# Kernel optimization log

Hardware: AMD Instinct MI355X
Metric: run time of the kernel (lower is better)

Reference implementation:

```python
import jax, jax.numpy as jnp
import numpy as np
import math

B, H, W = 32, 512, 512
BS = 8
QUALITY = 50.0  # __scale_quality(75) = 200 - 2*75


def _make_dctmtx(bs=BS):
    m = np.empty((bs, bs), dtype=np.float32)
    for j in range(bs):
        for i in range(bs):
            if i == 0:
                m[i, j] = 1.0 / math.sqrt(bs)
            else:
                m[i, j] = math.sqrt(2.0 / bs) * math.cos(math.pi * (2 * j + 1) * i / (2 * bs))
    return jnp.asarray(m)


def _make_quantize():
    qY = np.array([[16,11,10,16,24,40,51,61],[12,12,14,19,26,58,60,55],
                   [14,13,16,24,40,57,69,56],[14,17,22,29,51,87,80,62],
                   [18,22,37,56,68,109,103,77],[24,35,55,64,81,104,113,92],
                   [49,64,78,87,103,121,120,101],[72,92,95,98,112,100,103,99]], dtype=np.float32) / 255.0
    qC = np.array([[17,18,24,47,99,99,99,99],[18,21,26,66,99,99,99,99],
                   [24,26,56,99,99,99,99,99],[47,66,99,99,99,99,99,99],
                   [99,99,99,99,99,99,99,99],[99,99,99,99,99,99,99,99],
                   [99,99,99,99,99,99,99,99],[99,99,99,99,99,99,99,99]], dtype=np.float32) / 255.0
    return jnp.asarray(np.stack([qY, qC, qC], axis=0))


def setup_inputs() -> dict:
    key = jax.random.key(0)
    x = jax.random.uniform(key, (B, 3, H, W), dtype=jnp.float32)
    return {"input": x, "quantize": _make_quantize(), "dctmtx": _make_dctmtx()}


def reference(input, quantize, dctmtx):
    bs = BS
    b, c, h, w = input.shape
    dt = input.dtype
    rgb = 255.0 * input
    # rgb -> ycbcr (3x3 color transform, offset cb/cr by 128, clamp)
    xf = jnp.array([[0.299, 0.587, 0.114],
                    [-0.168735892, -0.331264108, 0.5],
                    [0.5, -0.418687589, -0.081312411]], dtype=dt)
    off = jnp.array([0.0, 128.0, 128.0], dtype=dt)[None, :, None, None]
    ycbcr = jnp.clip(jnp.einsum('bchw,kc->bkhw', rgb, xf) + off, 0.0, 255.0)
    # 2x2 chroma subsample: replace Cb/Cr by 2x2 block means (Y untouched)
    yc = ycbcr[:, :1]
    cc = ycbcr[:, 1:].reshape(b, 2, h // 2, 2, w // 2, 2)
    cm = jnp.mean(cc, axis=(3, 5), keepdims=True)
    cc = jnp.broadcast_to(cm, cc.shape).reshape(b, 2, h, w)
    sample = jnp.concatenate([yc, cc], axis=1) - 128.0
    # extract 8x8 blocks -> [b, h/bs, w/bs, 3, bs, bs]
    blocks = sample.reshape(b, 3, h // bs, bs, w // bs, bs).transpose(0, 2, 4, 1, 3, 5)
    # 2D DCT: D @ X @ D^T
    dcts = jnp.einsum('ij,bhwcjk,lk->bhwcil', dctmtx, blocks, dctmtx)
    # quality-scaled quant table (broadcasts [3,8,8] over blocks)
    q = jnp.round(jnp.clip(jnp.round((jnp.round(quantize * 255.0) * QUALITY + 50.0) / 100.0), 1.0, 255.0))
    comp = jnp.round(dcts / q)
    decomp = jnp.round(comp * jax.lax.stop_gradient(q))
    # IDCT: D^T @ X @ D
    idcts = jnp.einsum('ji,bhwcjk,kl->bhwcil', dctmtx, decomp, dctmtx)
    # merge blocks back -> [b,3,h,w]
    ycbcr2 = idcts.transpose(0, 3, 1, 4, 2, 5).reshape(b, 3, h, w) + 128.0
    # ycbcr -> rgb
    xf2 = jnp.array([[1.0, 0.0, 1.402],
                     [1.0, -0.344136286, -0.714136286],
                     [1.0, 1.772, 0.0]], dtype=dt)
    im = ycbcr2 - off
    rgb2 = jnp.clip(jnp.einsum('bchw,kc->bkhw', im, xf2), 0.0, 255.0)
    return jnp.round(rgb2) / 255.0
```

## Files before the change

kernel.cpp:

```cpp
#include <hip/hip_runtime.h>

#define IN_H 512
#define IN_W 512


__global__ __launch_bounds__(256, 2) void jpeg_kernel(
    const float* __restrict__ in, const float* __restrict__ qz,
    const float* __restrict__ dmtx, float* __restrict__ out)
{
    __shared__ __align__(16) unsigned char smem[62592];
    double* Ys   = (double*)(smem);
    double* CbS  = (double*)(smem + 16512);
    double* CrS  = (double*)(smem + 24832);
    double* T    = (double*)(smem + 33152);
    float*  U    = (float*) (smem + 33152);
    float*  Z    = (float*) (smem + 50560);
    double* qtab = (double*)(smem + 59264);
    float*  Df   = (float*) (smem + 62336);
    float* V[3]  = { (float*)(smem), (float*)(smem + 16512), (float*)(smem + 24832) };

    const int t   = threadIdx.x;
    const int blk = blockIdx.x;
    const int b   = blk >> 7;
    const int rr  = blk & 127;
    const int row0 = (rr >> 1) << 3;
    const int col0 = (rr & 1) << 8;
    const int chs = IN_H * IN_W;

    if (t < 192) {
        double v  = (double)qz[t];
        double t0 = rint(v * 255.0);
        double t1 = rint((t0 * 50.0 + 50.0) / 100.0);
        double q  = fmin(fmax(t1, 1.0), 255.0);
        qtab[2*t]   = 1.0 / q;
        qtab[2*t+1] = q;
    }
    if (t < 64) Df[t] = dmtx[t];

    const int s  = t >> 6;
    const int c4 = t & 63;
    {
        const int base = ((b*3) * IN_H + row0 + 2*s) * IN_W + col0 + 4*c4;
        float4 ra = *(const float4*)(in + base);
        float4 rb = *(const float4*)(in + base + IN_W);
        float4 ga = *(const float4*)(in + base + chs);
        float4 gb = *(const float4*)(in + base + chs + IN_W);
        float4 ba = *(const float4*)(in + base + 2*chs);
        float4 bb = *(const float4*)(in + base + 2*chs + IN_W);

        float rA[2][4] = {{ra.x,ra.y,ra.z,ra.w},{rb.x,rb.y,rb.z,rb.w}};
        float gA[2][4] = {{ga.x,ga.y,ga.z,ga.w},{gb.x,gb.y,gb.z,gb.w}};
        float bA[2][4] = {{ba.x,ba.y,ba.z,ba.w},{bb.x,bb.y,bb.z,bb.w}};

        double yv[2][4], cbv[2][4], crv[2][4];
        #pragma unroll
        for (int p = 0; p < 2; ++p) {
            #pragma unroll
            for (int k = 0; k < 4; ++k) {
                double R = 255.0 * (double)rA[p][k];
                double G = 255.0 * (double)gA[p][k];
                double B = 255.0 * (double)bA[p][k];
                double y  =  0.299*R + 0.587*G + 0.114*B;
                double cb = -0.168735892*R - 0.331264108*G + 0.5*B + 128.0;
                double cr =  0.5*R - 0.418687589*G - 0.081312411*B + 128.0;
                yv[p][k]  = fmin(fmax(y , 0.0), 255.0) - 128.0;
                cbv[p][k] = fmin(fmax(cb, 0.0), 255.0);
                crv[p][k] = fmin(fmax(cr, 0.0), 255.0);
            }
        }
        #pragma unroll
        for (int p = 0; p < 2; ++p) {
            double* yp = &Ys[(2*s+p)*258 + 4*c4];
            *(double2*)(yp)     = make_double2(yv[p][0], yv[p][1]);
            *(double2*)(yp + 2) = make_double2(yv[p][2], yv[p][3]);
        }
        double m0 = (cbv[0][0]+cbv[0][1]+cbv[1][0]+cbv[1][1])*0.25 - 128.0;
        double m1 = (cbv[0][2]+cbv[0][3]+cbv[1][2]+cbv[1][3])*0.25 - 128.0;
        *(double2*)&CbS[s*130 + 2*c4] = make_double2(m0, m1);
        double n0 = (crv[0][0]+crv[0][1]+crv[1][0]+crv[1][1])*0.25 - 128.0;
        double n1 = (crv[0][2]+crv[0][3]+crv[1][2]+crv[1][3])*0.25 - 128.0;
        *(double2*)&CrS[s*130 + 2*c4] = make_double2(n0, n1);
    }
    __syncthreads();

    float  dh[8][4];
    double dh64[8][4];
    #pragma unroll
    for (int l = 0; l < 8; ++l) {
        float4 d4 = *(const float4*)&Df[l*8];
        dh[l][0]=d4.x; dh[l][1]=d4.y; dh[l][2]=d4.z; dh[l][3]=d4.w;
        #pragma unroll
        for (int k = 0; k < 4; ++k) dh64[l][k] = (double)dh[l][k];
    }
    const int q8 = t >> 3;
    const int jl = t & 7;

    #pragma unroll
    for (int c = 0; c < 3; ++c) {
        {
            double x[8];
            if (c == 0) {
                const double* p = &Ys[jl*258 + q8*8];
                double2 a0 = *(const double2*)(p);
                double2 a1 = *(const double2*)(p+2);
                double2 a2 = *(const double2*)(p+4);
                double2 a3 = *(const double2*)(p+6);
                x[0]=a0.x; x[1]=a0.y; x[2]=a1.x; x[3]=a1.y;
                x[4]=a2.x; x[5]=a2.y; x[6]=a3.x; x[7]=a3.y;
            } else {
                const double* p = (c==1 ? CbS : CrS) + (jl>>1)*130 + q8*4;
                double2 a0 = *(const double2*)(p);
                double2 a1 = *(const double2*)(p+2);
                x[0]=a0.x; x[1]=a0.x; x[2]=a0.y; x[3]=a0.y;
                x[4]=a1.x; x[5]=a1.x; x[6]=a1.y; x[7]=a1.y;
            }
            double e[4], o[4];
            #pragma unroll
            for (int k = 0; k < 4; ++k) { e[k]=x[k]+x[7-k]; o[k]=x[k]-x[7-k]; }
            double* Tp = &T[q8*68 + jl*8];
            #pragma unroll
            for (int l = 0; l < 8; l += 2) {
                double te = dh64[l  ][0]*e[0] + dh64[l  ][1]*e[1] + dh64[l  ][2]*e[2] + dh64[l  ][3]*e[3];
                double to = dh64[l+1][0]*o[0] + dh64[l+1][1]*o[1] + dh64[l+1][2]*o[2] + dh64[l+1][3]*o[3];
                *(double2*)(Tp + l) = make_double2(te, to);
            }
        }
        __syncthreads();

        {
            const double* Tc = &T[q8*68 + jl];
            double tc[8];
            #pragma unroll
            for (int j2 = 0; j2 < 8; ++j2) tc[j2] = Tc[j2*8];
            double e2[4], o2[4];
            #pragma unroll
            for (int m = 0; m < 4; ++m) { e2[m]=tc[m]+tc[7-m]; o2[m]=tc[m]-tc[7-m]; }
            float* Zc = &Z[q8*68 + jl];
            #pragma unroll
            for (int i = 0; i < 8; ++i) {
                double acc;
                if ((i & 1) == 0)
                    acc = dh64[i][0]*e2[0]+dh64[i][1]*e2[1]+dh64[i][2]*e2[2]+dh64[i][3]*e2[3];
                else
                    acc = dh64[i][0]*o2[0]+dh64[i][1]*o2[1]+dh64[i][2]*o2[2]+dh64[i][3]*o2[3];
                double2 qe = *(const double2*)&qtab[2*(c*64 + i*8 + jl)];
                double comp = rint(acc * qe.x);
                Zc[i*8] = (float)(comp * qe.y);
            }
        }
        __syncthreads();

        {
            const float* Zp = &Z[q8*68 + jl*8];
            float4 z0 = *(const float4*)(Zp);
            float4 z1 = *(const float4*)(Zp+4);
            float zz[8] = {z0.x,z0.y,z0.z,z0.w,z1.x,z1.y,z1.z,z1.w};
            float se[4], so[4], uu[8];
            #pragma unroll
            for (int l2 = 0; l2 < 4; ++l2) {
                se[l2] = zz[0]*dh[0][l2] + zz[2]*dh[2][l2] + zz[4]*dh[4][l2] + zz[6]*dh[6][l2];
                so[l2] = zz[1]*dh[1][l2] + zz[3]*dh[3][l2] + zz[5]*dh[5][l2] + zz[7]*dh[7][l2];
            }
            #pragma unroll
            for (int l2 = 0; l2 < 4; ++l2) { uu[l2]=se[l2]+so[l2]; uu[7-l2]=se[l2]-so[l2]; }
            float* Upp = &U[q8*68 + jl*8];
            *(float4*)(Upp)   = make_float4(uu[0],uu[1],uu[2],uu[3]);
            *(float4*)(Upp+4) = make_float4(uu[4],uu[5],uu[6],uu[7]);
        }
        __syncthreads();

        {
            const float* Up2 = &U[q8*68 + jl];
            float uu[8];
            #pragma unroll
            for (int j2 = 0; j2 < 8; ++j2) uu[j2] = Up2[j2*8];
            float se[4], so[4];
            #pragma unroll
            for (int i2 = 0; i2 < 4; ++i2) {
                se[i2] = uu[0]*dh[0][i2] + uu[2]*dh[2][i2] + uu[4]*dh[4][i2] + uu[6]*dh[6][i2];
                so[i2] = uu[1]*dh[1][i2] + uu[3]*dh[3][i2] + uu[5]*dh[5][i2] + uu[7]*dh[7][i2];
            }
            float* Vc = V[c];
            #pragma unroll
            for (int i2 = 0; i2 < 4; ++i2) {
                Vc[i2*260     + q8*8 + jl] = se[i2] + so[i2];
                Vc[(7-i2)*260 + q8*8 + jl] = se[i2] - so[i2];
            }
        }
        __syncthreads();
    }

    {
        const int obase = ((b*3) * IN_H + row0 + 2*s) * IN_W + col0 + 4*c4;
        #pragma unroll
        for (int p = 0; p < 2; ++p) {
            const int roff = (2*s+p)*260 + 4*c4;
            float4 vy = *(const float4*)&V[0][roff];
            float4 vb = *(const float4*)&V[1][roff];
            float4 vr = *(const float4*)&V[2][roff];
            float yv2[4]={vy.x,vy.y,vy.z,vy.w};
            float cb2[4]={vb.x,vb.y,vb.z,vb.w};
            float cr2[4]={vr.x,vr.y,vr.z,vr.w};
            float R4[4],G4[4],B4[4];
            #pragma unroll
            for (int k = 0; k < 4; ++k) {
                float im0 = yv2[k] + 128.0f;
                float im1 = cb2[k];
                float im2 = cr2[k];
                float R = fminf(fmaxf(im0 + 1.402f*im2, 0.0f), 255.0f);
                float G = fminf(fmaxf(im0 - 0.344136286f*im1 - 0.714136286f*im2, 0.0f), 255.0f);
                float B = fminf(fmaxf(im0 + 1.772f*im1, 0.0f), 255.0f);
                R4[k] = rintf(R) * (1.0f/255.0f);
                G4[k] = rintf(G) * (1.0f/255.0f);
                B4[k] = rintf(B) * (1.0f/255.0f);
            }
            float* op = out + obase + p*IN_W;
            *(float4*)(op)         = make_float4(R4[0],R4[1],R4[2],R4[3]);
            *(float4*)(op + chs)   = make_float4(G4[0],G4[1],G4[2],G4[3]);
            *(float4*)(op + 2*chs) = make_float4(B4[0],B4[1],B4[2],B4[3]);
        }
    }
}

extern "C" void kernel_launch(void* const* d_in, const int* in_sizes, int n_in,
                              void* d_out, int out_size, void* d_ws, size_t ws_size,
                              hipStream_t stream) {
    (void)in_sizes; (void)n_in; (void)out_size; (void)d_ws; (void)ws_size;
    const float* in  = (const float*)d_in[0];
    const float* qz  = (const float*)d_in[1];
    const float* dm  = (const float*)d_in[2];
    float* out = (float*)d_out;
    dim3 grid(4096), blk(256);
    hipLaunchKernelGGL(jpeg_kernel, grid, blk, 0, stream, in, qz, dm, out);
}
```

Before: 195.3 us.

## Restructure JPEG DCT pipeline to cut shared memory and barriers, raise occupancy

```diff
diff --git a/kernel.cpp b/kernel.cpp
--- a/kernel.cpp
+++ b/kernel.cpp
@@ -4,20 +4,18 @@
 #define IN_W 512
 
 
-__global__ __launch_bounds__(256, 2) void jpeg_kernel(
+__global__ __launch_bounds__(256, 4) void jpeg_kernel(
     const float* __restrict__ in, const float* __restrict__ qz,
     const float* __restrict__ dmtx, float* __restrict__ out)
 {
-    __shared__ __align__(16) unsigned char smem[62592];
-    double* Ys   = (double*)(smem);
-    double* CbS  = (double*)(smem + 16512);
-    double* CrS  = (double*)(smem + 24832);
-    double* T    = (double*)(smem + 33152);
-    float*  U    = (float*) (smem + 33152);
-    float*  Z    = (float*) (smem + 50560);
-    double* qtab = (double*)(smem + 59264);
-    float*  Df   = (float*) (smem + 62336);
-    float* V[3]  = { (float*)(smem), (float*)(smem + 16512), (float*)(smem + 24832) };
+    __shared__ __align__(16) unsigned char smem[39168];
+    double*  Ys  = (double*) (smem);
+    double*  CbS = (double*) (smem + 17408);
+    double*  CrS = (double*) (smem + 22016);
+    float*   Zt  = (float*)  (smem + 26624);
+    double2* qt  = (double2*)(smem + 35328);
+    double*  Dd  = (double*) (smem + 38784);
+    float*   Dh  = (float*)  (smem + 39040);
 
     const int t   = threadIdx.x;
     const int blk = blockIdx.x;
@@ -28,25 +26,28 @@
     const int chs = IN_H * IN_W;
 
     if (t < 192) {
+        const int c = t >> 6, i = (t >> 3) & 7, l = t & 7;
         double v  = (double)qz[t];
-        double t0 = rint(v * 255.0);
-        double t1 = rint((t0 * 50.0 + 50.0) / 100.0);
+        double t1 = rint((rint(v * 255.0) * 50.0 + 50.0) / 100.0);
         double q  = fmin(fmax(t1, 1.0), 255.0);
-        qtab[2*t]   = 1.0 / q;
-        qtab[2*t+1] = q;
-    }
-    if (t < 64) Df[t] = dmtx[t];
+        qt[(c * 8 + l) * 9 + i] = make_double2(1.0 / q, q);
+    }
+    if (t < 32) {
+        float dv = dmtx[(t >> 2) * 8 + (t & 3)];
+        Dd[t] = (double)dv;
+        Dh[t] = dv;
+    }
 
     const int s  = t >> 6;
     const int c4 = t & 63;
     {
-        const int base = ((b*3) * IN_H + row0 + 2*s) * IN_W + col0 + 4*c4;
+        const int base = ((b * 3) * IN_H + row0 + 2 * s) * IN_W + col0 + 4 * c4;
         float4 ra = *(const float4*)(in + base);
         float4 rb = *(const float4*)(in + base + IN_W);
         float4 ga = *(const float4*)(in + base + chs);
         float4 gb = *(const float4*)(in + base + chs + IN_W);
-        float4 ba = *(const float4*)(in + base + 2*chs);
-        float4 bb = *(const float4*)(in + base + 2*chs + IN_W);
+        float4 ba = *(const float4*)(in + base + 2 * chs);
+        float4 bb = *(const float4*)(in + base + 2 * chs + IN_W);
 
         float rA[2][4] = {{ra.x,ra.y,ra.z,ra.w},{rb.x,rb.y,rb.z,rb.w}};
         float gA[2][4] = {{ga.x,ga.y,ga.z,ga.w},{gb.x,gb.y,gb.z,gb.w}};
@@ -68,157 +69,131 @@
                 crv[p][k] = fmin(fmax(cr, 0.0), 255.0);
             }
         }
+        const int tile = c4 >> 1, half = c4 & 1;
         #pragma unroll
         for (int p = 0; p < 2; ++p) {
-            double* yp = &Ys[(2*s+p)*258 + 4*c4];
+            double* yp = &Ys[tile * 68 + (2*s + p) * 8 + 4 * half];
             *(double2*)(yp)     = make_double2(yv[p][0], yv[p][1]);
             *(double2*)(yp + 2) = make_double2(yv[p][2], yv[p][3]);
         }
         double m0 = (cbv[0][0]+cbv[0][1]+cbv[1][0]+cbv[1][1])*0.25 - 128.0;
         double m1 = (cbv[0][2]+cbv[0][3]+cbv[1][2]+cbv[1][3])*0.25 - 128.0;
-        *(double2*)&CbS[s*130 + 2*c4] = make_double2(m0, m1);
+        *(double2*)&CbS[tile * 18 + s * 4 + 2 * half] = make_double2(m0, m1);
         double n0 = (crv[0][0]+crv[0][1]+crv[1][0]+crv[1][1])*0.25 - 128.0;
         double n1 = (crv[0][2]+crv[0][3]+crv[1][2]+crv[1][3])*0.25 - 128.0;
-        *(double2*)&CrS[s*130 + 2*c4] = make_double2(n0, n1);
+        *(double2*)&CrS[tile * 18 + s * 4 + 2 * half] = make_double2(n0, n1);
     }
     __syncthreads();
 
-    float  dh[8][4];
-    double dh64[8][4];
-    #pragma unroll
-    for (int l = 0; l < 8; ++l) {
-        float4 d4 = *(const float4*)&Df[l*8];
-        dh[l][0]=d4.x; dh[l][1]=d4.y; dh[l][2]=d4.z; dh[l][3]=d4.w;
-        #pragma unroll
-        for (int k = 0; k < 4; ++k) dh64[l][k] = (double)dh[l][k];
-    }
     const int q8 = t >> 3;
-    const int jl = t & 7;
+    const int l  = t & 7;
+    double dl0, dl1, dl2, dl3;
+    {
+        double2 dA = *(const double2*)&Dd[l * 4];
+        double2 dB = *(const double2*)&Dd[l * 4 + 2];
+        dl0 = dA.x; dl1 = dA.y; dl2 = dB.x; dl3 = dB.y;
+    }
+    const double sgn  = (l & 1) ? -1.0 : 1.0;
+    const double dl01 = dl0 + dl1, dl23 = dl2 + dl3;
+    float dcol[8];
+    {
+        const int   lc = (l < 4) ? l : 7 - l;
+        #pragma unroll
+        for (int k = 0; k < 8; ++k) {
+            float dv = Dh[k * 4 + lc];
+            dcol[k] = ((k & 1) && (l >= 4)) ? -dv : dv;
+        }
+    }
+
+    float acc[3][8];
 
     #pragma unroll
     for (int c = 0; c < 3; ++c) {
-        {
-            double x[8];
-            if (c == 0) {
-                const double* p = &Ys[jl*258 + q8*8];
+        double tj[8];
+        if (c == 0) {
+            const double* base = &Ys[q8 * 68];
+            #pragma unroll
+            for (int j = 0; j < 8; ++j) {
+                const double* p = base + j * 8;
                 double2 a0 = *(const double2*)(p);
-                double2 a1 = *(const double2*)(p+2);
-                double2 a2 = *(const double2*)(p+4);
-                double2 a3 = *(const double2*)(p+6);
-                x[0]=a0.x; x[1]=a0.y; x[2]=a1.x; x[3]=a1.y;
-                x[4]=a2.x; x[5]=a2.y; x[6]=a3.x; x[7]=a3.y;
-            } else {
-                const double* p = (c==1 ? CbS : CrS) + (jl>>1)*130 + q8*4;
-                double2 a0 = *(const double2*)(p);
-                double2 a1 = *(const double2*)(p+2);
-                x[0]=a0.x; x[1]=a0.x; x[2]=a0.y; x[3]=a0.y;
-                x[4]=a1.x; x[5]=a1.x; x[6]=a1.y; x[7]=a1.y;
+                double2 a1 = *(const double2*)(p + 2);
+                double2 a2 = *(const double2*)(p + 4);
+                double2 a3 = *(const double2*)(p + 6);
+                double v0 = fma(sgn, a3.y, a0.x);
+                double v1 = fma(sgn, a3.x, a0.y);
+                double v2 = fma(sgn, a2.y, a1.x);
+                double v3 = fma(sgn, a2.x, a1.y);
+                tj[j] = dl0*v0 + dl1*v1 + dl2*v2 + dl3*v3;
             }
-            double e[4], o[4];
+        } else {
+            const double* base = ((c == 1) ? CbS : CrS) + q8 * 18;
             #pragma unroll
-            for (int k = 0; k < 4; ++k) { e[k]=x[k]+x[7-k]; o[k]=x[k]-x[7-k]; }
-            double* Tp = &T[q8*68 + jl*8];
-            #pragma unroll
-            for (int l = 0; l < 8; l += 2) {
-                double te = dh64[l  ][0]*e[0] + dh64[l  ][1]*e[1] + dh64[l  ][2]*e[2] + dh64[l  ][3]*e[3];
-                double to = dh64[l+1][0]*o[0] + dh64[l+1][1]*o[1] + dh64[l+1][2]*o[2] + dh64[l+1][3]*o[3];
-                *(double2*)(Tp + l) = make_double2(te, to);
+            for (int j2 = 0; j2 < 4; ++j2) {
+                double2 a0 = *(const double2*)(base + j2 * 4);
+                double2 a1 = *(const double2*)(base + j2 * 4 + 2);
+                double u = dl01 * fma(sgn, a1.y, a0.x) + dl23 * fma(sgn, a1.x, a0.y);
+                tj[2*j2] = u; tj[2*j2 + 1] = u;
             }
         }
+        double e2[4], o2[4];
+        #pragma unroll
+        for (int m = 0; m < 4; ++m) { e2[m] = tj[m] + tj[7-m]; o2[m] = tj[m] - tj[7-m]; }
+
+        float zo[8];
+        const double2* dd2  = (const double2*)Dd;
+        const double2* qrow = &qt[(c * 8 + l) * 9];
+        #pragma unroll
+        for (int i = 0; i < 8; ++i) {
+            double2 dA = dd2[i * 2], dB = dd2[i * 2 + 1];
+            double a64 = (i & 1)
+                ? dA.x*o2[0] + dA.y*o2[1] + dB.x*o2[2] + dB.y*o2[3]
+                : dA.x*e2[0] + dA.y*e2[1] + dB.x*e2[2] + dB.y*e2[3];
+            double2 qe = qrow[i];
+            zo[i] = (float)(rint(a64 * qe.x) * qe.y);
+        }
+        float* zp = &Zt[q8 * 68 + l * 8];
+        *(float4*)(zp)     = make_float4(zo[0], zo[1], zo[2], zo[3]);
+        *(float4*)(zp + 4) = make_float4(zo[4], zo[5], zo[6], zo[7]);
         __syncthreads();
 
-        {
-            const double* Tc = &T[q8*68 + jl];
-            double tc[8];
-            #pragma unroll
-            for (int j2 = 0; j2 < 8; ++j2) tc[j2] = Tc[j2*8];
-            double e2[4], o2[4];
-            #pragma unroll
-            for (int m = 0; m < 4; ++m) { e2[m]=tc[m]+tc[7-m]; o2[m]=tc[m]-tc[7-m]; }
-            float* Zc = &Z[q8*68 + jl];
-            #pragma unroll
-            for (int i = 0; i < 8; ++i) {
-                double acc;
-                if ((i & 1) == 0)
-                    acc = dh64[i][0]*e2[0]+dh64[i][1]*e2[1]+dh64[i][2]*e2[2]+dh64[i][3]*e2[3];
-                else
-                    acc = dh64[i][0]*o2[0]+dh64[i][1]*o2[1]+dh64[i][2]*o2[2]+dh64[i][3]*o2[3];
-                double2 qe = *(const double2*)&qtab[2*(c*64 + i*8 + jl)];
-                double comp = rint(acc * qe.x);
-                Zc[i*8] = (float)(comp * qe.y);
-            }
-        }
-        __syncthreads();
-
-        {
-            const float* Zp = &Z[q8*68 + jl*8];
-            float4 z0 = *(const float4*)(Zp);
-            float4 z1 = *(const float4*)(Zp+4);
-            float zz[8] = {z0.x,z0.y,z0.z,z0.w,z1.x,z1.y,z1.z,z1.w};
-            float se[4], so[4], uu[8];
-            #pragma unroll
-            for (int l2 = 0; l2 < 4; ++l2) {
-                se[l2] = zz[0]*dh[0][l2] + zz[2]*dh[2][l2] + zz[4]*dh[4][l2] + zz[6]*dh[6][l2];
-                so[l2] = zz[1]*dh[1][l2] + zz[3]*dh[3][l2] + zz[5]*dh[5][l2] + zz[7]*dh[7][l2];
-            }
-            #pragma unroll
-            for (int l2 = 0; l2 < 4; ++l2) { uu[l2]=se[l2]+so[l2]; uu[7-l2]=se[l2]-so[l2]; }
-            float* Upp = &U[q8*68 + jl*8];
-            *(float4*)(Upp)   = make_float4(uu[0],uu[1],uu[2],uu[3]);
-            *(float4*)(Upp+4) = make_float4(uu[4],uu[5],uu[6],uu[7]);
-        }
-        __syncthreads();
-
-        {
-            const float* Up2 = &U[q8*68 + jl];
-            float uu[8];
-            #pragma unroll
-            for (int j2 = 0; j2 < 8; ++j2) uu[j2] = Up2[j2*8];
-            float se[4], so[4];
-            #pragma unroll
-            for (int i2 = 0; i2 < 4; ++i2) {
-                se[i2] = uu[0]*dh[0][i2] + uu[2]*dh[2][i2] + uu[4]*dh[4][i2] + uu[6]*dh[6][i2];
-                so[i2] = uu[1]*dh[1][i2] + uu[3]*dh[3][i2] + uu[5]*dh[5][i2] + uu[7]*dh[7][i2];
-            }
-            float* Vc = V[c];
-            #pragma unroll
-            for (int i2 = 0; i2 < 4; ++i2) {
-                Vc[i2*260     + q8*8 + jl] = se[i2] + so[i2];
-                Vc[(7-i2)*260 + q8*8 + jl] = se[i2] - so[i2];
-            }
-        }
-        __syncthreads();
-    }
-
-    {
-        const int obase = ((b*3) * IN_H + row0 + 2*s) * IN_W + col0 + 4*c4;
-        #pragma unroll
-        for (int p = 0; p < 2; ++p) {
-            const int roff = (2*s+p)*260 + 4*c4;
-            float4 vy = *(const float4*)&V[0][roff];
-            float4 vb = *(const float4*)&V[1][roff];
-            float4 vr = *(const float4*)&V[2][roff];
-            float yv2[4]={vy.x,vy.y,vy.z,vy.w};
-            float cb2[4]={vb.x,vb.y,vb.z,vb.w};
-            float cr2[4]={vr.x,vr.y,vr.z,vr.w};
-            float R4[4],G4[4],B4[4];
-            #pragma unroll
-            for (int k = 0; k < 4; ++k) {
-                float im0 = yv2[k] + 128.0f;
-                float im1 = cb2[k];
-                float im2 = cr2[k];
-                float R = fminf(fmaxf(im0 + 1.402f*im2, 0.0f), 255.0f);
-                float G = fminf(fmaxf(im0 - 0.344136286f*im1 - 0.714136286f*im2, 0.0f), 255.0f);
-                float B = fminf(fmaxf(im0 + 1.772f*im1, 0.0f), 255.0f);
-                R4[k] = rintf(R) * (1.0f/255.0f);
-                G4[k] = rintf(G) * (1.0f/255.0f);
-                B4[k] = rintf(B) * (1.0f/255.0f);
-            }
-            float* op = out + obase + p*IN_W;
-            *(float4*)(op)         = make_float4(R4[0],R4[1],R4[2],R4[3]);
-            *(float4*)(op + chs)   = make_float4(G4[0],G4[1],G4[2],G4[3]);
-            *(float4*)(op + 2*chs) = make_float4(B4[0],B4[1],B4[2],B4[3]);
-        }
+        float w[8] = {0,0,0,0,0,0,0,0};
+        const float* zb = &Zt[q8 * 68];
+        #pragma unroll
+        for (int k = 0; k < 8; ++k) {
+            float4 z0 = *(const float4*)(zb + k * 8);
+            float4 z1 = *(const float4*)(zb + k * 8 + 4);
+            float dk = dcol[k];
+            w[0] += z0.x*dk; w[1] += z0.y*dk; w[2] += z0.z*dk; w[3] += z0.w*dk;
+            w[4] += z1.x*dk; w[5] += z1.y*dk; w[6] += z1.z*dk; w[7] += z1.w*dk;
+        }
+        const float4* dh4 = (const float4*)Dh;
+        float se[4] = {0,0,0,0}, so[4] = {0,0,0,0};
+        #pragma unroll
+        for (int j = 0; j < 8; j += 2) {
+            float4 de = dh4[j], dq = dh4[j + 1];
+            se[0] += de.x*w[j];   se[1] += de.y*w[j];   se[2] += de.z*w[j];   se[3] += de.w*w[j];
+            so[0] += dq.x*w[j+1]; so[1] += dq.y*w[j+1]; so[2] += dq.z*w[j+1]; so[3] += dq.w*w[j+1];
+        }
+        #pragma unroll
+        for (int i2 = 0; i2 < 4; ++i2) {
+            acc[c][i2]     = se[i2] + so[i2];
+            acc[c][7 - i2] = se[i2] - so[i2];
+        }
+        if (c < 2) __syncthreads();
+    }
+
+    #pragma unroll
+    for (int i = 0; i < 8; ++i) {
+        float im0 = acc[0][i] + 128.0f;
+        float im1 = acc[1][i];
+        float im2 = acc[2][i];
+        float R  = fminf(fmaxf(im0 + 1.402f*im2, 0.0f), 255.0f);
+        float G  = fminf(fmaxf(im0 - 0.344136286f*im1 - 0.714136286f*im2, 0.0f), 255.0f);
+        float Bv = fminf(fmaxf(im0 + 1.772f*im1, 0.0f), 255.0f);
+        const int base = ((b * 3) * IN_H + row0 + i) * IN_W + col0 + t;
+        out[base]           = rintf(R)  * (1.0f/255.0f);
+        out[base + chs]     = rintf(G)  * (1.0f/255.0f);
+        out[base + 2*chs]   = rintf(Bv) * (1.0f/255.0f);
     }
 }
 
```

After: 380.9 us. +95.1%, slower.
